# Kernel tuning notes

Measured on AMD Instinct MI355X. Metric: run time of the kernel, lower is better.

Reference implementation:

```python
import jax, jax.numpy as jnp
import numpy as np

HID = 10     # hidden_size
IN = 4       # input_size
OUT = 4
P = 5        # predict_ahead


def setup_inputs() -> dict:
    key = jax.random.key(0)
    ks = jax.random.split(key, 7)
    B, T = 16384, 100
    x = jax.random.normal(ks[0], (B, T, IN), dtype=jnp.float32)
    s = 1.0 / np.sqrt(HID)  # PyTorch default uniform init bound
    W_ih = jax.random.uniform(ks[1], (4 * HID, IN), jnp.float32, -s, s)
    W_hh = jax.random.uniform(ks[2], (4 * HID, HID), jnp.float32, -s, s)
    b_ih = jax.random.uniform(ks[3], (4 * HID,), jnp.float32, -s, s)
    b_hh = jax.random.uniform(ks[4], (4 * HID,), jnp.float32, -s, s)
    W_lin = jax.random.uniform(ks[5], (OUT, HID), jnp.float32, -s, s)
    b_lin = jax.random.uniform(ks[6], (OUT,), jnp.float32, -s, s)
    return {"x": x, "W_ih": W_ih, "W_hh": W_hh, "b_ih": b_ih,
            "b_hh": b_hh, "W_lin": W_lin, "b_lin": b_lin}


def _lstm_cell(xt, h, c, W_ih, W_hh, b_ih, b_hh):
    # PyTorch gate order: i, f, g, o
    gates = xt @ W_ih.T + h @ W_hh.T + (b_ih + b_hh)  # [B, 4H]
    i, f, g, o = jnp.split(gates, 4, axis=-1)
    c_new = jax.nn.sigmoid(f) * c + jax.nn.sigmoid(i) * jnp.tanh(g)
    h_new = jax.nn.sigmoid(o) * jnp.tanh(c_new)
    return h_new, c_new


def reference(x, W_ih, W_hh, b_ih, b_hh, W_lin, b_lin):
    B, T, _ = x.shape
    Tp = T - P + 1  # number of outer time steps
    h0 = jnp.zeros((B, HID), x.dtype)
    c0 = jnp.zeros((B, HID), x.dtype)
    xs = jnp.transpose(x[:, :Tp, :], (1, 0, 2))  # [Tp, B, IN]

    def step(carry, xt):
        h, c = carry
        h, c = _lstm_cell(xt, h, c, W_ih, W_hh, b_ih, b_hh)
        y = h @ W_lin.T + b_lin  # [B, OUT]
        outs = [y]
        h_a, c_a = h, c
        for _ in range(P - 1):
            h_a, c_a = _lstm_cell(y, h_a, c_a, W_ih, W_hh, b_ih, b_hh)
            y = h_a @ W_lin.T + b_lin
            outs.append(y)
        return (h, c), jnp.stack(outs, axis=1)  # [B, P, OUT]

    (h, c), ys = jax.lax.scan(step, (h0, c0), xs)  # ys: [Tp, B, P, OUT]
    final_output = jnp.transpose(ys, (1, 0, 2, 3))  # [B, Tp, P, OUT]
    return final_output, c[None]  # c_t: [num_layers=1, B, HID]
```

## Files before the change

### kernel.cpp

```cpp
#include <hip/hip_runtime.h>


#define HIDN 10
#define INPN 4
#define OUTN 4
#define PN   5
#define TN   100
#define TPN  96
#define BN   16384
#define GPB  24

typedef float v2f __attribute__((ext_vector_type(2)));

#define PIN(x) asm volatile("" : "+v"(x))

__device__ __forceinline__ float rcpf_(float v) { return __builtin_amdgcn_rcpf(v); }
__device__ __forceinline__ float e2_(float v)   { return __builtin_amdgcn_exp2f(v); }
__device__ __forceinline__ float sig2_(float g)  { return rcpf_(1.0f + e2_(-g)); }
__device__ __forceinline__ float tanh2_(float g) { return fmaf(-2.0f, rcpf_(1.0f + e2_(g)), 1.0f); }

#define K2L2E 2.88539008177792681472f

__global__ __launch_bounds__(256, 1) void lstm_ar_kernel(
    const float* __restrict__ x,
    const float* __restrict__ W_ih,
    const float* __restrict__ W_hh,
    const float* __restrict__ b_ih,
    const float* __restrict__ b_hh,
    const float* __restrict__ W_lin,
    const float* __restrict__ b_lin,
    float* __restrict__ out)
{
    __shared__ __align__(16) float s_h[GPB][PN][20];

    const int tid = threadIdx.x;
    const int wid = tid >> 6;
    const int wl  = tid & 63;
    const int grp = wl / 10;
    const int u   = wl - grp * 10;
    const int slot  = wid * 6 + grp;
    const int batch = blockIdx.x * GPB + slot;
    if (grp >= 6 || batch >= BN) return;

    const float L2E = 1.44269504088896340736f;
    const float rs[4] = { L2E, L2E, 2.0f * L2E, L2E };

    v2f  wm2[4][5];
    v2f  wc2[4][5];
    v2f  wih2[4][2];
    float bm[4], br[4];
    #pragma unroll
    for (int r = 0; r < 4; ++r) {
        const int j = u + r * 10;
        float wmr[HIDN], wihr[INPN];
        #pragma unroll
        for (int k = 0; k < HIDN; ++k) wmr[k] = W_hh[j * HIDN + k];
        #pragma unroll
        for (int q = 0; q < INPN; ++q) wihr[q] = W_ih[j * INPN + q];
        float bmr = b_ih[j] + b_hh[j];
        float brr = bmr;
        #pragma unroll
        for (int q = 0; q < INPN; ++q) brr += wihr[q] * b_lin[q];
        #pragma unroll
        for (int k = 0; k < HIDN; ++k) {
            float wck = wmr[k];
            #pragma unroll
            for (int q = 0; q < INPN; ++q) wck += wihr[q] * W_lin[q * HIDN + k];
            if (k & 1) {
                wm2[r][k >> 1].y = wmr[k] * rs[r];
                wc2[r][k >> 1].y = wck    * rs[r];
            } else {
                wm2[r][k >> 1].x = wmr[k] * rs[r];
                wc2[r][k >> 1].x = wck    * rs[r];
            }
        }
        #pragma unroll
        for (int q = 0; q < INPN; ++q) {
            if (q & 1) wih2[r][q >> 1].y = wihr[q] * rs[r];
            else       wih2[r][q >> 1].x = wihr[q] * rs[r];
        }
        bm[r] = bmr * rs[r];
        br[r] = brr * rs[r];
    }

    const int pmine = u >> 1;
    const int opair = (u & 1) * 2;
    v2f yl0[5], yl1[5];
    #pragma unroll
    for (int k = 0; k < HIDN; k += 2) {
        yl0[k >> 1] = v2f{ W_lin[opair * HIDN + k],        W_lin[opair * HIDN + k + 1] };
        yl1[k >> 1] = v2f{ W_lin[(opair + 1) * HIDN + k],  W_lin[(opair + 1) * HIDN + k + 1] };
    }
    float yb0 = b_lin[opair];
    float yb1 = b_lin[opair + 1];

    #pragma unroll
    for (int r = 0; r < 4; ++r) {
        #pragma unroll
        for (int k = 0; k < 5; ++k) { PIN(wm2[r][k]); PIN(wc2[r][k]); }
        PIN(wih2[r][0]); PIN(wih2[r][1]);
        PIN(bm[r]); PIN(br[r]);
    }
    #pragma unroll
    for (int k = 0; k < 5; ++k) { PIN(yl0[k]); PIN(yl1[k]); }
    PIN(yb0); PIN(yb1);

    const float* xb   = x + (long)batch * TN * INPN;
    float*       outb = out + (long)batch * TPN * PN * OUTN;

    v2f hm2[5];
    float cm = 0.0f;
    #pragma unroll
    for (int k = 0; k < 5; ++k) hm2[k] = v2f{0.0f, 0.0f};

    float4 xcur = *(const float4*)xb;
    for (int t = 0; t < TPN; ++t) {
        float4 xnext = *(const float4*)(xb + (t + 1) * INPN);

        v2f xa = v2f{xcur.x, xcur.y}, xc = v2f{xcur.z, xcur.w};
        float g[4];
        #pragma unroll
        for (int r = 0; r < 4; ++r) {
            v2f acc = v2f{bm[r], 0.0f};
            acc = __builtin_elementwise_fma(wih2[r][0], xa, acc);
            acc = __builtin_elementwise_fma(wih2[r][1], xc, acc);
            #pragma unroll
            for (int k = 0; k < 5; ++k)
                acc = __builtin_elementwise_fma(wm2[r][k], hm2[k], acc);
            g[r] = acc.x + acc.y;
        }
        {
            float iv = sig2_(g[0]), fv = sig2_(g[1]), gv = tanh2_(g[2]), ov = sig2_(g[3]);
            cm = fmaf(fv, cm, iv * gv);
            float hn = ov * tanh2_(cm * K2L2E);
            s_h[slot][0][u] = hn;
        }
        __builtin_amdgcn_wave_barrier();
        {
            float4 a = *(const float4*)&s_h[slot][0][0];
            float4 b = *(const float4*)&s_h[slot][0][4];
            float2 c = *(const float2*)&s_h[slot][0][8];
            hm2[0] = v2f{a.x, a.y}; hm2[1] = v2f{a.z, a.w};
            hm2[2] = v2f{b.x, b.y}; hm2[3] = v2f{b.z, b.w};
            hm2[4] = v2f{c.x, c.y};
        }

        v2f hr2[5];
        #pragma unroll
        for (int k = 0; k < 5; ++k) hr2[k] = hm2[k];
        float cr = cm;
        #pragma unroll
        for (int p = 1; p < PN; ++p) {
            #pragma unroll
            for (int r = 0; r < 4; ++r) {
                v2f acc = v2f{br[r], 0.0f};
                #pragma unroll
                for (int k = 0; k < 5; ++k)
                    acc = __builtin_elementwise_fma(wc2[r][k], hr2[k], acc);
                g[r] = acc.x + acc.y;
            }
            float iv = sig2_(g[0]), fv = sig2_(g[1]), gv = tanh2_(g[2]), ov = sig2_(g[3]);
            cr = fmaf(fv, cr, iv * gv);
            float hn = ov * tanh2_(cr * K2L2E);
            s_h[slot][p][u] = hn;
            __builtin_amdgcn_wave_barrier();
            if (p < PN - 1) {
                float4 a = *(const float4*)&s_h[slot][p][0];
                float4 b = *(const float4*)&s_h[slot][p][4];
                float2 c = *(const float2*)&s_h[slot][p][8];
                hr2[0] = v2f{a.x, a.y}; hr2[1] = v2f{a.z, a.w};
                hr2[2] = v2f{b.x, b.y}; hr2[3] = v2f{b.z, b.w};
                hr2[4] = v2f{c.x, c.y};
            }
        }

        {
            float4 a = *(const float4*)&s_h[slot][pmine][0];
            float4 b = *(const float4*)&s_h[slot][pmine][4];
            float2 c = *(const float2*)&s_h[slot][pmine][8];
            v2f h0 = v2f{a.x, a.y}, h1 = v2f{a.z, a.w};
            v2f h2 = v2f{b.x, b.y}, h3 = v2f{b.z, b.w};
            v2f h4 = v2f{c.x, c.y};
            v2f a0 = v2f{yb0, 0.0f}, a1 = v2f{yb1, 0.0f};
            a0 = __builtin_elementwise_fma(yl0[0], h0, a0);
            a1 = __builtin_elementwise_fma(yl1[0], h0, a1);
            a0 = __builtin_elementwise_fma(yl0[1], h1, a0);
            a1 = __builtin_elementwise_fma(yl1[1], h1, a1);
            a0 = __builtin_elementwise_fma(yl0[2], h2, a0);
            a1 = __builtin_elementwise_fma(yl1[2], h2, a1);
            a0 = __builtin_elementwise_fma(yl0[3], h3, a0);
            a1 = __builtin_elementwise_fma(yl1[3], h3, a1);
            a0 = __builtin_elementwise_fma(yl0[4], h4, a0);
            a1 = __builtin_elementwise_fma(yl1[4], h4, a1);
            float2 yv; yv.x = a0.x + a0.y; yv.y = a1.x + a1.y;
            *(float2*)(outb + t * PN * OUTN + 2 * u) = yv;
        }

        xcur = xnext;
    }

    out[(long)BN * TPN * PN * OUTN + (long)batch * HIDN + u] = cm;
}

extern "C" void kernel_launch(void* const* d_in, const int* in_sizes, int n_in,
                              void* d_out, int out_size, void* d_ws, size_t ws_size,
                              hipStream_t stream) {
    const float* x     = (const float*)d_in[0];
    const float* W_ih  = (const float*)d_in[1];
    const float* W_hh  = (const float*)d_in[2];
    const float* b_ih  = (const float*)d_in[3];
    const float* b_hh  = (const float*)d_in[4];
    const float* W_lin = (const float*)d_in[5];
    const float* b_lin = (const float*)d_in[6];
    float* out = (float*)d_out;

    const int grid = (BN + GPB - 1) / GPB;
    lstm_ar_kernel<<<grid, 256, 0, stream>>>(x, W_ih, W_hh, b_ih, b_hh, W_lin, b_lin, out);
}
```

Before: 198.9 us.

## Fold the main-step W_hh product into combined weights via an x-minus-y correction

The main LSTM step now reuses the rollout's combined weights (W_hh + W_ih·W_lin) and feeds the input as x minus the previous step's linear output. That linear output is kept in shared memory and seeded with b_lin. This removes the separate W_hh register set and its biases, which cuts register pressure, and launch bounds are raised to allow 3 blocks per CU so all blocks can be resident at once. The cost is an extra shared-memory round trip for y, an extra wave barrier per step, and slightly different floating-point rounding from the algebraic rearrangement.

Result: faster. 185.7 us (-6.7%).

```diff
diff --git a/kernel.cpp b/kernel.cpp
--- a/kernel.cpp
+++ b/kernel.cpp
@@ -21,7 +21,7 @@
 
 #define K2L2E 2.88539008177792681472f
 
-__global__ __launch_bounds__(256, 1) void lstm_ar_kernel(
+__global__ __launch_bounds__(256, 3) void lstm_ar_kernel(
     const float* __restrict__ x,
     const float* __restrict__ W_ih,
     const float* __restrict__ W_hh,
@@ -32,6 +32,7 @@
     float* __restrict__ out)
 {
     __shared__ __align__(16) float s_h[GPB][PN][20];
+    __shared__ __align__(16) float s_y[GPB][4];
 
     const int tid = threadIdx.x;
     const int wid = tid >> 6;
@@ -45,42 +46,32 @@
     const float L2E = 1.44269504088896340736f;
     const float rs[4] = { L2E, L2E, 2.0f * L2E, L2E };
 
-    v2f  wm2[4][5];
     v2f  wc2[4][5];
     v2f  wih2[4][2];
-    float bm[4], br[4];
+    v2f  br2[4];
     #pragma unroll
     for (int r = 0; r < 4; ++r) {
         const int j = u + r * 10;
-        float wmr[HIDN], wihr[INPN];
-        #pragma unroll
-        for (int k = 0; k < HIDN; ++k) wmr[k] = W_hh[j * HIDN + k];
+        float wihr[INPN];
         #pragma unroll
         for (int q = 0; q < INPN; ++q) wihr[q] = W_ih[j * INPN + q];
-        float bmr = b_ih[j] + b_hh[j];
-        float brr = bmr;
+        float brr = b_ih[j] + b_hh[j];
         #pragma unroll
         for (int q = 0; q < INPN; ++q) brr += wihr[q] * b_lin[q];
         #pragma unroll
         for (int k = 0; k < HIDN; ++k) {
-            float wck = wmr[k];
+            float wck = W_hh[j * HIDN + k];
             #pragma unroll
             for (int q = 0; q < INPN; ++q) wck += wihr[q] * W_lin[q * HIDN + k];
-            if (k & 1) {
-                wm2[r][k >> 1].y = wmr[k] * rs[r];
-                wc2[r][k >> 1].y = wck    * rs[r];
-            } else {
-                wm2[r][k >> 1].x = wmr[k] * rs[r];
-                wc2[r][k >> 1].x = wck    * rs[r];
-            }
+            if (k & 1) wc2[r][k >> 1].y = wck * rs[r];
+            else       wc2[r][k >> 1].x = wck * rs[r];
         }
         #pragma unroll
         for (int q = 0; q < INPN; ++q) {
             if (q & 1) wih2[r][q >> 1].y = wihr[q] * rs[r];
             else       wih2[r][q >> 1].x = wihr[q] * rs[r];
         }
-        bm[r] = bmr * rs[r];
-        br[r] = brr * rs[r];
+        br2[r] = v2f{ brr * rs[r], 0.0f };
     }
 
     const int pmine = u >> 1;
@@ -91,72 +82,76 @@
         yl0[k >> 1] = v2f{ W_lin[opair * HIDN + k],        W_lin[opair * HIDN + k + 1] };
         yl1[k >> 1] = v2f{ W_lin[(opair + 1) * HIDN + k],  W_lin[(opair + 1) * HIDN + k + 1] };
     }
-    float yb0 = b_lin[opair];
-    float yb1 = b_lin[opair + 1];
+    v2f ybv0 = v2f{ b_lin[opair],     0.0f };
+    v2f ybv1 = v2f{ b_lin[opair + 1], 0.0f };
 
     #pragma unroll
     for (int r = 0; r < 4; ++r) {
         #pragma unroll
-        for (int k = 0; k < 5; ++k) { PIN(wm2[r][k]); PIN(wc2[r][k]); }
-        PIN(wih2[r][0]); PIN(wih2[r][1]);
-        PIN(bm[r]); PIN(br[r]);
+        for (int k = 0; k < 5; ++k) PIN(wc2[r][k]);
+        PIN(wih2[r][0]); PIN(wih2[r][1]); PIN(br2[r]);
     }
     #pragma unroll
     for (int k = 0; k < 5; ++k) { PIN(yl0[k]); PIN(yl1[k]); }
-    PIN(yb0); PIN(yb1);
+    PIN(ybv0); PIN(ybv1);
+
+    s_h[slot][0][u] = 0.0f;
+    if (u < 4) s_y[slot][u] = b_lin[u];
+    __builtin_amdgcn_wave_barrier();
 
     const float* xb   = x + (long)batch * TN * INPN;
     float*       outb = out + (long)batch * TPN * PN * OUTN;
 
-    v2f hm2[5];
     float cm = 0.0f;
-    #pragma unroll
-    for (int k = 0; k < 5; ++k) hm2[k] = v2f{0.0f, 0.0f};
-
     float4 xcur = *(const float4*)xb;
     for (int t = 0; t < TPN; ++t) {
         float4 xnext = *(const float4*)(xb + (t + 1) * INPN);
 
-        v2f xa = v2f{xcur.x, xcur.y}, xc = v2f{xcur.z, xcur.w};
+        v2f h2[5];
         float g[4];
-        #pragma unroll
-        for (int r = 0; r < 4; ++r) {
-            v2f acc = v2f{bm[r], 0.0f};
-            acc = __builtin_elementwise_fma(wih2[r][0], xa, acc);
-            acc = __builtin_elementwise_fma(wih2[r][1], xc, acc);
+
+        {
+            float4 yp = *(const float4*)&s_y[slot][0];
+            float4 a  = *(const float4*)&s_h[slot][0][0];
+            float4 b  = *(const float4*)&s_h[slot][0][4];
+            float2 c2 = *(const float2*)&s_h[slot][0][8];
+            h2[0] = v2f{a.x, a.y}; h2[1] = v2f{a.z, a.w};
+            h2[2] = v2f{b.x, b.y}; h2[3] = v2f{b.z, b.w};
+            h2[4] = v2f{c2.x, c2.y};
+            v2f dxa = v2f{xcur.x - yp.x, xcur.y - yp.y};
+            v2f dxc = v2f{xcur.z - yp.z, xcur.w - yp.w};
             #pragma unroll
-            for (int k = 0; k < 5; ++k)
-                acc = __builtin_elementwise_fma(wm2[r][k], hm2[k], acc);
-            g[r] = acc.x + acc.y;
-        }
-        {
+            for (int r = 0; r < 4; ++r) {
+                v2f acc = br2[r];
+                acc = __builtin_elementwise_fma(wih2[r][0], dxa, acc);
+                acc = __builtin_elementwise_fma(wih2[r][1], dxc, acc);
+                #pragma unroll
+                for (int k = 0; k < 5; ++k)
+                    acc = __builtin_elementwise_fma(wc2[r][k], h2[k], acc);
+                g[r] = acc.x + acc.y;
+            }
             float iv = sig2_(g[0]), fv = sig2_(g[1]), gv = tanh2_(g[2]), ov = sig2_(g[3]);
             cm = fmaf(fv, cm, iv * gv);
             float hn = ov * tanh2_(cm * K2L2E);
             s_h[slot][0][u] = hn;
         }
         __builtin_amdgcn_wave_barrier();
-        {
-            float4 a = *(const float4*)&s_h[slot][0][0];
-            float4 b = *(const float4*)&s_h[slot][0][4];
-            float2 c = *(const float2*)&s_h[slot][0][8];
-            hm2[0] = v2f{a.x, a.y}; hm2[1] = v2f{a.z, a.w};
-            hm2[2] = v2f{b.x, b.y}; hm2[3] = v2f{b.z, b.w};
-            hm2[4] = v2f{c.x, c.y};
-        }
-
-        v2f hr2[5];
-        #pragma unroll
-        for (int k = 0; k < 5; ++k) hr2[k] = hm2[k];
+
         float cr = cm;
         #pragma unroll
         for (int p = 1; p < PN; ++p) {
+            float4 a  = *(const float4*)&s_h[slot][p - 1][0];
+            float4 b  = *(const float4*)&s_h[slot][p - 1][4];
+            float2 c2 = *(const float2*)&s_h[slot][p - 1][8];
+            h2[0] = v2f{a.x, a.y}; h2[1] = v2f{a.z, a.w};
+            h2[2] = v2f{b.x, b.y}; h2[3] = v2f{b.z, b.w};
+            h2[4] = v2f{c2.x, c2.y};
             #pragma unroll
             for (int r = 0; r < 4; ++r) {
-                v2f acc = v2f{br[r], 0.0f};
+                v2f acc = br2[r];
                 #pragma unroll
                 for (int k = 0; k < 5; ++k)
-                    acc = __builtin_elementwise_fma(wc2[r][k], hr2[k], acc);
+                    acc = __builtin_elementwise_fma(wc2[r][k], h2[k], acc);
                 g[r] = acc.x + acc.y;
             }
             float iv = sig2_(g[0]), fv = sig2_(g[1]), gv = tanh2_(g[2]), ov = sig2_(g[3]);
@@ -164,37 +159,31 @@
             float hn = ov * tanh2_(cr * K2L2E);
             s_h[slot][p][u] = hn;
             __builtin_amdgcn_wave_barrier();
-            if (p < PN - 1) {
-                float4 a = *(const float4*)&s_h[slot][p][0];
-                float4 b = *(const float4*)&s_h[slot][p][4];
-                float2 c = *(const float2*)&s_h[slot][p][8];
-                hr2[0] = v2f{a.x, a.y}; hr2[1] = v2f{a.z, a.w};
-                hr2[2] = v2f{b.x, b.y}; hr2[3] = v2f{b.z, b.w};
-                hr2[4] = v2f{c.x, c.y};
-            }
         }
 
         {
-            float4 a = *(const float4*)&s_h[slot][pmine][0];
-            float4 b = *(const float4*)&s_h[slot][pmine][4];
-            float2 c = *(const float2*)&s_h[slot][pmine][8];
-            v2f h0 = v2f{a.x, a.y}, h1 = v2f{a.z, a.w};
-            v2f h2 = v2f{b.x, b.y}, h3 = v2f{b.z, b.w};
-            v2f h4 = v2f{c.x, c.y};
-            v2f a0 = v2f{yb0, 0.0f}, a1 = v2f{yb1, 0.0f};
+            float4 a  = *(const float4*)&s_h[slot][pmine][0];
+            float4 b  = *(const float4*)&s_h[slot][pmine][4];
+            float2 c2 = *(const float2*)&s_h[slot][pmine][8];
+            v2f h0 = v2f{a.x, a.y},  h1 = v2f{a.z, a.w};
+            v2f h3 = v2f{b.x, b.y},  h4 = v2f{b.z, b.w};
+            v2f h5 = v2f{c2.x, c2.y};
+            v2f a0 = ybv0, a1 = ybv1;
             a0 = __builtin_elementwise_fma(yl0[0], h0, a0);
             a1 = __builtin_elementwise_fma(yl1[0], h0, a1);
             a0 = __builtin_elementwise_fma(yl0[1], h1, a0);
             a1 = __builtin_elementwise_fma(yl1[1], h1, a1);
-            a0 = __builtin_elementwise_fma(yl0[2], h2, a0);
-            a1 = __builtin_elementwise_fma(yl1[2], h2, a1);
-            a0 = __builtin_elementwise_fma(yl0[3], h3, a0);
-            a1 = __builtin_elementwise_fma(yl1[3], h3, a1);
-            a0 = __builtin_elementwise_fma(yl0[4], h4, a0);
-            a1 = __builtin_elementwise_fma(yl1[4], h4, a1);
+            a0 = __builtin_elementwise_fma(yl0[2], h3, a0);
+            a1 = __builtin_elementwise_fma(yl1[2], h3, a1);
+            a0 = __builtin_elementwise_fma(yl0[3], h4, a0);
+            a1 = __builtin_elementwise_fma(yl1[3], h4, a1);
+            a0 = __builtin_elementwise_fma(yl0[4], h5, a0);
+            a1 = __builtin_elementwise_fma(yl1[4], h5, a1);
             float2 yv; yv.x = a0.x + a0.y; yv.y = a1.x + a1.y;
             *(float2*)(outb + t * PN * OUTN + 2 * u) = yv;
-        }
+            if (u < 2) *(float2*)&s_y[slot][2 * u] = yv;
+        }
+        __builtin_amdgcn_wave_barrier();
 
         xcur = xnext;
     }
```
